# Kernel optimization log

Hardware: AMD Instinct MI355X
Metric: run time of the kernel (lower is better)

## Reference

```python
import jax, jax.numpy as jnp
import numpy as np

N, VW, DW, VP, DP, H, M = 1024, 50000, 300, 50, 100, 512, 256


def _run_dir(x, Wih, Whh, b, reverse):
    # Single-direction LSTM over [n, in] -> [n, H]. PyTorch gate order i,f,g,o.
    Hh = Whh.shape[1]
    def step(carry, xt):
        h, c = carry
        z = xt @ Wih.T + h @ Whh.T + b  # [4H]
        i, f, g, o = jnp.split(z, 4, axis=-1)
        c = jax.nn.sigmoid(f) * c + jax.nn.sigmoid(i) * jnp.tanh(g)
        h = jax.nn.sigmoid(o) * jnp.tanh(c)
        return (h, c), h
    init = (jnp.zeros((Hh,), x.dtype), jnp.zeros((Hh,), x.dtype))
    _, hs = jax.lax.scan(step, init, x, reverse=reverse)
    return hs


def setup_inputs() -> dict:
    key = jax.random.key(0)
    ks = jax.random.split(key, 24)
    s = 0.05  # small init to keep tanh/sigmoid unsaturated
    d = {
        "word_idx": jax.random.randint(ks[0], (N,), 0, VW, dtype=jnp.int32),
        "pos_idx": jax.random.randint(ks[1], (N,), 0, VP, dtype=jnp.int32),
        "word_emb": jax.random.normal(ks[2], (VW, DW), jnp.float32) * s,
        "pos_emb": jax.random.normal(ks[3], (VP, DP), jnp.float32) * s,
        "wih0f": jax.random.normal(ks[4], (4 * H, DW + DP), jnp.float32) * s,
        "whh0f": jax.random.normal(ks[5], (4 * H, H), jnp.float32) * s,
        "b0f": jax.random.normal(ks[6], (4 * H,), jnp.float32) * s,
        "wih0r": jax.random.normal(ks[7], (4 * H, DW + DP), jnp.float32) * s,
        "whh0r": jax.random.normal(ks[8], (4 * H, H), jnp.float32) * s,
        "b0r": jax.random.normal(ks[9], (4 * H,), jnp.float32) * s,
        "wih1f": jax.random.normal(ks[10], (4 * H, 2 * H), jnp.float32) * s,
        "whh1f": jax.random.normal(ks[11], (4 * H, H), jnp.float32) * s,
        "b1f": jax.random.normal(ks[12], (4 * H,), jnp.float32) * s,
        "wih1r": jax.random.normal(ks[13], (4 * H, 2 * H), jnp.float32) * s,
        "whh1r": jax.random.normal(ks[14], (4 * H, H), jnp.float32) * s,
        "b1r": jax.random.normal(ks[15], (4 * H,), jnp.float32) * s,
        "W1": jax.random.normal(ks[16], (M, 4 * H), jnp.float32) * s,
        "bmlp1": jax.random.normal(ks[17], (M,), jnp.float32) * s,
        "w2": jax.random.normal(ks[18], (1, M), jnp.float32) * s,
        "b2": jax.random.normal(ks[19], (1,), jnp.float32) * s,
    }
    return d


def reference(word_idx, pos_idx, word_emb, pos_emb,
              wih0f, whh0f, b0f, wih0r, whh0r, b0r,
              wih1f, whh1f, b1f, wih1r, whh1r, b1r,
              W1, bmlp1, w2, b2):
    # Embed words + pos, concat -> [n, 400]
    x = jnp.concatenate([word_emb[word_idx], pos_emb[pos_idx]], axis=1)
    # 2-layer bidirectional LSTM encoder (batch of 1 squeezed away, as in the module)
    h0 = jnp.concatenate([_run_dir(x, wih0f, whh0f, b0f, False),
                          _run_dir(x, wih0r, whh0r, b0r, True)], axis=1)   # [n, 2H]
    h1 = jnp.concatenate([_run_dir(h0, wih1f, whh1f, b1f, False),
                          _run_dir(h0, wih1r, whh1r, b1r, True)], axis=1)  # [n, 2H]
    # Pairwise MLP score: MLP(concat(h_i, h_j)). Split W1 into head/dep halves so the
    # big GEMM is done once per token instead of once per pair (same math).
    twoH = h1.shape[1]
    a = h1 @ W1[:, :twoH].T            # [n, M], contribution of h_i
    bpart = h1 @ W1[:, twoH:].T        # [n, M], contribution of h_j
    hidden = jnp.tanh(a[:, None, :] + bpart[None, :, :] + bmlp1)  # [n, n, M]
    scores = hidden @ w2[0] + b2[0]    # [n, n]
    return scores
```

## Files before the change

kernel.cpp:

```cpp
#include <hip/hip_runtime.h>
#include <hip/hip_bf16.h>

#define HID   512
#define SEQ   1024
#define GATES 2048

__device__ __forceinline__ float sigm(float x) {
    return 1.f / (1.f + __expf(-x));
}
__device__ __forceinline__ float tanh_fast(float x) {
    float ax = fabsf(x);
    float e  = __expf(-2.f * ax);
    float t  = (1.f - e) * __builtin_amdgcn_rcpf(1.f + e);
    return copysignf(t, x);
}
__device__ __forceinline__ float bcast(float v, int l) {
    return __uint_as_float((unsigned)__builtin_amdgcn_readlane((int)__float_as_uint(v), l));
}

__global__ void embed_kernel(const int* __restrict__ wi, const int* __restrict__ pi,
                             const float* __restrict__ we, const float* __restrict__ pe,
                             float* __restrict__ x) {
    int i = blockIdx.x;
    int t = threadIdx.x;
    const float* w = we + (size_t)wi[i] * 300;
    const float* p = pe + (size_t)pi[i] * 100;
    float* xo = x + (size_t)i * 400;
    for (int c = t; c < 300; c += 128) xo[c]       = w[c];
    for (int c = t; c < 100; c += 128) xo[300 + c] = p[c];
}

__global__ __launch_bounds__(256)
void gemm_bias(const float* __restrict__ A, const float* __restrict__ B,
               const float* __restrict__ bias, float* __restrict__ C,
               int M, int N, int K, int lda, int ldb, int ldc) {
    __shared__ __align__(16) float As[16 * 68];
    __shared__ __align__(16) float Bs[16 * 68];
    const int tid  = threadIdx.x;
    const int bn   = blockIdx.x, bm = blockIdx.y;
    const int tj   = tid & 15, ti = tid >> 4;
    const int lrow = tid >> 2;
    const int lk4  = (tid & 3) << 2;
    float acc[4][4] = {};

    for (int kt = 0; kt < K; kt += 16) {
        float4 av = *(const float4*)(A + (size_t)(bm * 64 + lrow) * lda + kt + lk4);
        float4 bv = *(const float4*)(B + (size_t)(bn * 64 + lrow) * ldb + kt + lk4);
        As[(lk4 + 0) * 68 + lrow] = av.x; As[(lk4 + 1) * 68 + lrow] = av.y;
        As[(lk4 + 2) * 68 + lrow] = av.z; As[(lk4 + 3) * 68 + lrow] = av.w;
        Bs[(lk4 + 0) * 68 + lrow] = bv.x; Bs[(lk4 + 1) * 68 + lrow] = bv.y;
        Bs[(lk4 + 2) * 68 + lrow] = bv.z; Bs[(lk4 + 3) * 68 + lrow] = bv.w;
        __syncthreads();
        #pragma unroll
        for (int k = 0; k < 16; ++k) {
            float4 a4 = *(const float4*)&As[k * 68 + ti * 4];
            float4 b4 = *(const float4*)&Bs[k * 68 + tj * 4];
            acc[0][0] = fmaf(a4.x, b4.x, acc[0][0]); acc[0][1] = fmaf(a4.x, b4.y, acc[0][1]);
            acc[0][2] = fmaf(a4.x, b4.z, acc[0][2]); acc[0][3] = fmaf(a4.x, b4.w, acc[0][3]);
            acc[1][0] = fmaf(a4.y, b4.x, acc[1][0]); acc[1][1] = fmaf(a4.y, b4.y, acc[1][1]);
            acc[1][2] = fmaf(a4.y, b4.z, acc[1][2]); acc[1][3] = fmaf(a4.y, b4.w, acc[1][3]);
            acc[2][0] = fmaf(a4.z, b4.x, acc[2][0]); acc[2][1] = fmaf(a4.z, b4.y, acc[2][1]);
            acc[2][2] = fmaf(a4.z, b4.z, acc[2][2]); acc[2][3] = fmaf(a4.z, b4.w, acc[2][3]);
            acc[3][0] = fmaf(a4.w, b4.x, acc[3][0]); acc[3][1] = fmaf(a4.w, b4.y, acc[3][1]);
            acc[3][2] = fmaf(a4.w, b4.z, acc[3][2]); acc[3][3] = fmaf(a4.w, b4.w, acc[3][3]);
        }
        __syncthreads();
    }
    const int n0 = bn * 64 + tj * 4;
    float bb0 = 0.f, bb1 = 0.f, bb2 = 0.f, bb3 = 0.f;
    if (bias) { bb0 = bias[n0]; bb1 = bias[n0 + 1]; bb2 = bias[n0 + 2]; bb3 = bias[n0 + 3]; }
    #pragma unroll
    for (int i = 0; i < 4; ++i) {
        float4 o;
        o.x = acc[i][0] + bb0; o.y = acc[i][1] + bb1;
        o.z = acc[i][2] + bb2; o.w = acc[i][3] + bb3;
        *(float4*)(C + (size_t)(bm * 64 + ti * 4 + i) * ldc + n0) = o;
    }
}

__global__ __launch_bounds__(512)
void lstm_layer(const float* __restrict__ Zf, const float* __restrict__ Zr,
                const float* __restrict__ WhhF, const float* __restrict__ WhhR,
                unsigned long long* __restrict__ Hpair,
                float* __restrict__ Hout,
                unsigned tagBase) {
    const int dir = blockIdx.x >> 5;
    const int wg  = blockIdx.x & 31;
    const float* __restrict__ Z   = dir ? Zr   : Zf;
    const float* __restrict__ Whh = dir ? WhhR : WhhF;
    const int colOff = dir ? HID : 0;

    const int tid  = threadIdx.x;
    const int wave = tid >> 6;
    const int lane = tid & 63;
    const int g    = lane >> 4;
    const int jj   = lane & 15;
    const int grow = g * HID + wg * 16 + jj;

    float w[64];
    {
        const float4* wp = (const float4*)(Whh + (size_t)grow * HID + wave * 64);
        #pragma unroll
        for (int q = 0; q < 16; ++q) {
            float4 v = wp[q];
            w[4 * q] = v.x; w[4 * q + 1] = v.y; w[4 * q + 2] = v.z; w[4 * q + 3] = v.w;
        }
    }

    __shared__ float part[2][8 * 65];
    float cval = 0.f;

    for (int s = 0; s < SEQ; ++s) {
        const int t = dir ? (SEQ - 1 - s) : s;

        float zin = 0.f;
        if (wave == 0) zin = Z[(size_t)t * GATES + grow];

        float acc = 0.f;
        if (s > 0) {
            const int tp = dir ? (t + 1) : (t - 1);
            const unsigned expTag = tagBase + (unsigned)s - 1u;
            const unsigned long long* hp = Hpair + (size_t)tp * (2 * HID) + colOff + wave * 64;
            unsigned long long v;
            for (;;) {
                v = __hip_atomic_load(hp + lane, __ATOMIC_RELAXED, __HIP_MEMORY_SCOPE_AGENT);
                if (__all((unsigned)(v >> 32) == expTag)) break;
            }
            float hv = __uint_as_float((unsigned)v);
            float a0 = 0.f, a1 = 0.f, a2 = 0.f, a3 = 0.f;
            #pragma unroll
            for (int m = 0; m < 64; m += 4) {
                a0 = fmaf(w[m + 0], bcast(hv, m + 0), a0);
                a1 = fmaf(w[m + 1], bcast(hv, m + 1), a1);
                a2 = fmaf(w[m + 2], bcast(hv, m + 2), a2);
                a3 = fmaf(w[m + 3], bcast(hv, m + 3), a3);
            }
            acc = (a0 + a1) + (a2 + a3);
        }
        part[s & 1][wave * 65 + lane] = acc;
        __syncthreads();

        if (wave == 0) {
            const float* pp = part[s & 1];
            float r = zin;
            #pragma unroll
            for (int c = 0; c < 8; ++c) r += pp[c * 65 + lane];
            float zi = __shfl(r, jj);
            float zf = __shfl(r, 16 + jj);
            float zg = __shfl(r, 32 + jj);
            float zo = __shfl(r, 48 + jj);
            if (lane < 16) {
                float ig = sigm(zi), fg = sigm(zf), gg = tanh_fast(zg), og = sigm(zo);
                cval = fg * cval + ig * gg;
                float hv = og * tanh_fast(cval);
                const size_t oidx = (size_t)t * (2 * HID) + colOff + wg * 16 + lane;
                unsigned long long pk = ((unsigned long long)(tagBase + (unsigned)s) << 32)
                                      | (unsigned long long)__float_as_uint(hv);
                __hip_atomic_store(Hpair + oidx, pk, __ATOMIC_RELAXED, __HIP_MEMORY_SCOPE_AGENT);
                Hout[oidx] = hv;
            }
        }
    }
}

__global__ __launch_bounds__(256)
void pairwise_kernel(const float* __restrict__ Ah, const float* __restrict__ Bd,
                     const float* __restrict__ w2, const float* __restrict__ b2,
                     float* __restrict__ out) {
    __shared__ __align__(16) float at[16 * 260];
    __shared__ __align__(16) float bt[16 * 260];
    __shared__ __align__(16) float wl[256];
    const int tid = threadIdx.x;
    const int i0 = blockIdx.y * 16, j0 = blockIdx.x * 16;
    for (int u = tid; u < 16 * 256; u += 256) {
        int r = u >> 8, m = u & 255;
        at[r * 260 + m] = Ah[(size_t)(i0 + r) * 256 + m];
        bt[r * 260 + m] = Bd[(size_t)(j0 + r) * 256 + m];
    }
    wl[tid] = w2[tid];
    __syncthreads();
    const int tj = tid & 15, ti = tid >> 4;
    float acc = b2[0];
    #pragma unroll 2
    for (int m = 0; m < 256; m += 4) {
        float4 a4 = *(const float4*)&at[ti * 260 + m];
        float4 b4 = *(const float4*)&bt[tj * 260 + m];
        float4 w4 = *(const float4*)&wl[m];
        acc += tanh_fast(a4.x + b4.x) * w4.x;
        acc += tanh_fast(a4.y + b4.y) * w4.y;
        acc += tanh_fast(a4.z + b4.z) * w4.z;
        acc += tanh_fast(a4.w + b4.w) * w4.w;
    }
    out[(size_t)(i0 + ti) * 1024 + (j0 + tj)] = acc;
}

extern "C" void kernel_launch(void* const* d_in, const int* in_sizes, int n_in,
                              void* d_out, int out_size, void* d_ws, size_t ws_size,
                              hipStream_t stream) {
    const int*   wi    = (const int*)  d_in[0];
    const int*   pi    = (const int*)  d_in[1];
    const float* we    = (const float*)d_in[2];
    const float* pe    = (const float*)d_in[3];
    const float* wih0f = (const float*)d_in[4];
    const float* whh0f = (const float*)d_in[5];
    const float* b0f   = (const float*)d_in[6];
    const float* wih0r = (const float*)d_in[7];
    const float* whh0r = (const float*)d_in[8];
    const float* b0r   = (const float*)d_in[9];
    const float* wih1f = (const float*)d_in[10];
    const float* whh1f = (const float*)d_in[11];
    const float* b1f   = (const float*)d_in[12];
    const float* wih1r = (const float*)d_in[13];
    const float* whh1r = (const float*)d_in[14];
    const float* b1r   = (const float*)d_in[15];
    const float* W1    = (const float*)d_in[16];
    const float* bmlp1 = (const float*)d_in[17];
    const float* w2    = (const float*)d_in[18];
    const float* b2    = (const float*)d_in[19];
    float* out = (float*)d_out;

    char* wsb = (char*)d_ws;
    float* x  = (float*)(wsb + 512);
    float* zA = x  + (size_t)1024 * 400;
    float* zB = zA + (size_t)1024 * 2048;
    float* h0 = zB + (size_t)1024 * 2048;
    float* h1 = h0 + (size_t)1024 * 1024;
    float* aH = h1 + (size_t)1024 * 1024;
    float* bD = aH + (size_t)1024 * 256;
    unsigned long long* Hpair = (unsigned long long*)(bD + (size_t)1024 * 256);

    embed_kernel<<<dim3(1024), dim3(128), 0, stream>>>(wi, pi, we, pe, x);

    gemm_bias<<<dim3(32, 16), dim3(256), 0, stream>>>(x, wih0f, b0f, zA, 1024, 2048, 400, 400, 400, 2048);
    gemm_bias<<<dim3(32, 16), dim3(256), 0, stream>>>(x, wih0r, b0r, zB, 1024, 2048, 400, 400, 400, 2048);

    lstm_layer<<<dim3(64), dim3(512), 0, stream>>>(zA, zB, whh0f, whh0r, Hpair, h0, 1u);

    gemm_bias<<<dim3(32, 16), dim3(256), 0, stream>>>(h0, wih1f, b1f, zA, 1024, 2048, 1024, 1024, 1024, 2048);
    gemm_bias<<<dim3(32, 16), dim3(256), 0, stream>>>(h0, wih1r, b1r, zB, 1024, 2048, 1024, 1024, 1024, 2048);

    lstm_layer<<<dim3(64), dim3(512), 0, stream>>>(zA, zB, whh1f, whh1r, Hpair, h1, 8192u);

    gemm_bias<<<dim3(4, 16), dim3(256), 0, stream>>>(h1, W1,        bmlp1,   aH, 1024, 256, 1024, 1024, 2048, 256);
    gemm_bias<<<dim3(4, 16), dim3(256), 0, stream>>>(h1, W1 + 1024, nullptr, bD, 1024, 256, 1024, 1024, 2048, 256);

    pairwise_kernel<<<dim3(64, 64), dim3(256), 0, stream>>>(aH, bD, w2, b2, out);
}
```

Before: 3.492 ms.

## Merge paired GEMM launches, enlarge M tile, and parallelize LSTM gate nonlinearities

The GEMM kernel now handles two weight matrices in one launch using blockIdx.z, and its tile grows to 128 rows so each thread accumulates 8x4 outputs. This halves the number of GEMM launches and raises arithmetic intensity per shared-memory load. Separately, the LSTM cell now applies sigmoid or tanh on all 64 lanes before the shuffles instead of four serial nonlinearities on 16 lanes, which shortens the per-step critical path. The costs are more registers per thread and fewer blocks per GEMM launch.

```diff
diff --git a/kernel.cpp b/kernel.cpp
--- a/kernel.cpp
+++ b/kernel.cpp
@@ -31,38 +31,49 @@
 }
 
 __global__ __launch_bounds__(256)
-void gemm_bias(const float* __restrict__ A, const float* __restrict__ B,
-               const float* __restrict__ bias, float* __restrict__ C,
-               int M, int N, int K, int lda, int ldb, int ldc) {
-    __shared__ __align__(16) float As[16 * 68];
+void gemm_bias2(const float* __restrict__ A,
+                const float* __restrict__ B0, const float* __restrict__ bias0, float* __restrict__ C0,
+                const float* __restrict__ B1, const float* __restrict__ bias1, float* __restrict__ C1,
+                int M, int N, int K, int lda, int ldb, int ldc) {
+    const float* B    = blockIdx.z ? B1    : B0;
+    const float* bias = blockIdx.z ? bias1 : bias0;
+    float*       C    = blockIdx.z ? C1    : C0;
+
+    __shared__ __align__(16) float As[16 * 132];
     __shared__ __align__(16) float Bs[16 * 68];
     const int tid  = threadIdx.x;
     const int bn   = blockIdx.x, bm = blockIdx.y;
     const int tj   = tid & 15, ti = tid >> 4;
-    const int lrow = tid >> 2;
-    const int lk4  = (tid & 3) << 2;
-    float acc[4][4] = {};
+    const int arow = tid >> 1;
+    const int ak8  = (tid & 1) * 8;
+    const int brow = tid >> 2;
+    const int bk4  = (tid & 3) * 4;
+    float acc[8][4] = {};
 
     for (int kt = 0; kt < K; kt += 16) {
-        float4 av = *(const float4*)(A + (size_t)(bm * 64 + lrow) * lda + kt + lk4);
-        float4 bv = *(const float4*)(B + (size_t)(bn * 64 + lrow) * ldb + kt + lk4);
-        As[(lk4 + 0) * 68 + lrow] = av.x; As[(lk4 + 1) * 68 + lrow] = av.y;
-        As[(lk4 + 2) * 68 + lrow] = av.z; As[(lk4 + 3) * 68 + lrow] = av.w;
-        Bs[(lk4 + 0) * 68 + lrow] = bv.x; Bs[(lk4 + 1) * 68 + lrow] = bv.y;
-        Bs[(lk4 + 2) * 68 + lrow] = bv.z; Bs[(lk4 + 3) * 68 + lrow] = bv.w;
+        float4 a0 = *(const float4*)(A + (size_t)(bm * 128 + arow) * lda + kt + ak8);
+        float4 a1 = *(const float4*)(A + (size_t)(bm * 128 + arow) * lda + kt + ak8 + 4);
+        float4 bv = *(const float4*)(B + (size_t)(bn * 64 + brow) * ldb + kt + bk4);
+        As[(ak8 + 0) * 132 + arow] = a0.x; As[(ak8 + 1) * 132 + arow] = a0.y;
+        As[(ak8 + 2) * 132 + arow] = a0.z; As[(ak8 + 3) * 132 + arow] = a0.w;
+        As[(ak8 + 4) * 132 + arow] = a1.x; As[(ak8 + 5) * 132 + arow] = a1.y;
+        As[(ak8 + 6) * 132 + arow] = a1.z; As[(ak8 + 7) * 132 + arow] = a1.w;
+        Bs[(bk4 + 0) * 68 + brow] = bv.x; Bs[(bk4 + 1) * 68 + brow] = bv.y;
+        Bs[(bk4 + 2) * 68 + brow] = bv.z; Bs[(bk4 + 3) * 68 + brow] = bv.w;
         __syncthreads();
         #pragma unroll
         for (int k = 0; k < 16; ++k) {
-            float4 a4 = *(const float4*)&As[k * 68 + ti * 4];
+            float4 x0 = *(const float4*)&As[k * 132 + ti * 8];
+            float4 x1 = *(const float4*)&As[k * 132 + ti * 8 + 4];
             float4 b4 = *(const float4*)&Bs[k * 68 + tj * 4];
-            acc[0][0] = fmaf(a4.x, b4.x, acc[0][0]); acc[0][1] = fmaf(a4.x, b4.y, acc[0][1]);
-            acc[0][2] = fmaf(a4.x, b4.z, acc[0][2]); acc[0][3] = fmaf(a4.x, b4.w, acc[0][3]);
-            acc[1][0] = fmaf(a4.y, b4.x, acc[1][0]); acc[1][1] = fmaf(a4.y, b4.y, acc[1][1]);
-            acc[1][2] = fmaf(a4.y, b4.z, acc[1][2]); acc[1][3] = fmaf(a4.y, b4.w, acc[1][3]);
-            acc[2][0] = fmaf(a4.z, b4.x, acc[2][0]); acc[2][1] = fmaf(a4.z, b4.y, acc[2][1]);
-            acc[2][2] = fmaf(a4.z, b4.z, acc[2][2]); acc[2][3] = fmaf(a4.z, b4.w, acc[2][3]);
-            acc[3][0] = fmaf(a4.w, b4.x, acc[3][0]); acc[3][1] = fmaf(a4.w, b4.y, acc[3][1]);
-            acc[3][2] = fmaf(a4.w, b4.z, acc[3][2]); acc[3][3] = fmaf(a4.w, b4.w, acc[3][3]);
+            const float av[8] = {x0.x, x0.y, x0.z, x0.w, x1.x, x1.y, x1.z, x1.w};
+            #pragma unroll
+            for (int i = 0; i < 8; ++i) {
+                acc[i][0] = fmaf(av[i], b4.x, acc[i][0]);
+                acc[i][1] = fmaf(av[i], b4.y, acc[i][1]);
+                acc[i][2] = fmaf(av[i], b4.z, acc[i][2]);
+                acc[i][3] = fmaf(av[i], b4.w, acc[i][3]);
+            }
         }
         __syncthreads();
     }
@@ -70,11 +81,11 @@
     float bb0 = 0.f, bb1 = 0.f, bb2 = 0.f, bb3 = 0.f;
     if (bias) { bb0 = bias[n0]; bb1 = bias[n0 + 1]; bb2 = bias[n0 + 2]; bb3 = bias[n0 + 3]; }
     #pragma unroll
-    for (int i = 0; i < 4; ++i) {
+    for (int i = 0; i < 8; ++i) {
         float4 o;
         o.x = acc[i][0] + bb0; o.y = acc[i][1] + bb1;
         o.z = acc[i][2] + bb2; o.w = acc[i][3] + bb3;
-        *(float4*)(C + (size_t)(bm * 64 + ti * 4 + i) * ldc + n0) = o;
+        *(float4*)(C + (size_t)(bm * 128 + ti * 8 + i) * ldc + n0) = o;
     }
 }
 
@@ -145,12 +156,12 @@
             float r = zin;
             #pragma unroll
             for (int c = 0; c < 8; ++c) r += pp[c * 65 + lane];
-            float zi = __shfl(r, jj);
-            float zf = __shfl(r, 16 + jj);
-            float zg = __shfl(r, 32 + jj);
-            float zo = __shfl(r, 48 + jj);
+            float nl = (g == 2) ? tanh_fast(r) : sigm(r);
+            float ig = __shfl(nl, jj);
+            float fg = __shfl(nl, 16 + jj);
+            float gg = __shfl(nl, 32 + jj);
+            float og = __shfl(nl, 48 + jj);
             if (lane < 16) {
-                float ig = sigm(zi), fg = sigm(zf), gg = tanh_fast(zg), og = sigm(zo);
                 cval = fg * cval + ig * gg;
                 float hv = og * tanh_fast(cval);
                 const size_t oidx = (size_t)t * (2 * HID) + colOff + wg * 16 + lane;
@@ -231,18 +242,18 @@
 
     embed_kernel<<<dim3(1024), dim3(128), 0, stream>>>(wi, pi, we, pe, x);
 
-    gemm_bias<<<dim3(32, 16), dim3(256), 0, stream>>>(x, wih0f, b0f, zA, 1024, 2048, 400, 400, 400, 2048);
-    gemm_bias<<<dim3(32, 16), dim3(256), 0, stream>>>(x, wih0r, b0r, zB, 1024, 2048, 400, 400, 400, 2048);
+    gemm_bias2<<<dim3(32, 8, 2), dim3(256), 0, stream>>>(
+        x, wih0f, b0f, zA, wih0r, b0r, zB, 1024, 2048, 400, 400, 400, 2048);
 
     lstm_layer<<<dim3(64), dim3(512), 0, stream>>>(zA, zB, whh0f, whh0r, Hpair, h0, 1u);
 
-    gemm_bias<<<dim3(32, 16), dim3(256), 0, stream>>>(h0, wih1f, b1f, zA, 1024, 2048, 1024, 1024, 1024, 2048);
-    gemm_bias<<<dim3(32, 16), dim3(256), 0, stream>>>(h0, wih1r, b1r, zB, 1024, 2048, 1024, 1024, 1024, 2048);
+    gemm_bias2<<<dim3(32, 8, 2), dim3(256), 0, stream>>>(
+        h0, wih1f, b1f, zA, wih1r, b1r, zB, 1024, 2048, 1024, 1024, 1024, 2048);
 
     lstm_layer<<<dim3(64), dim3(512), 0, stream>>>(zA, zB, whh1f, whh1r, Hpair, h1, 8192u);
 
-    gemm_bias<<<dim3(4, 16), dim3(256), 0, stream>>>(h1, W1,        bmlp1,   aH, 1024, 256, 1024, 1024, 2048, 256);
-    gemm_bias<<<dim3(4, 16), dim3(256), 0, stream>>>(h1, W1 + 1024, nullptr, bD, 1024, 256, 1024, 1024, 2048, 256);
+    gemm_bias2<<<dim3(4, 8, 2), dim3(256), 0, stream>>>(
+        h1, W1, bmlp1, aH, W1 + 1024, nullptr, bD, 1024, 256, 1024, 1024, 2048, 256);
 
     pairwise_kernel<<<dim3(64, 64), dim3(256), 0, stream>>>(aH, bD, w2, b2, out);
 }
```

New measurement: 3.461 ms. About the same (-0.9%).
